# Kernel tuning notes

Hardware: AMD Instinct MI355X
Metric: run time of the kernel (lower is better)

The kernel has to match this reference:

```python
import jax, jax.numpy as jnp
import numpy as np

BLOCK = 8
MAN = 7  # bf16-style mantissa bits


def _ste(x, qx):
    # straight-through estimator: forward = qx, backward = identity
    return x + jax.lax.stop_gradient(qx - x)


def bf16_q(x):
    # fake-quantize to bfloat16 (exp=8, man=7, round-to-nearest)
    return _ste(x, x.astype(jnp.bfloat16).astype(x.dtype))


def bfp_q(x, axis):
    # block floating point: shared exponent per block of 8 along `axis`,
    # 7 mantissa bits relative to floor(log2(max|block|)).
    xm = jnp.moveaxis(x, axis, -1)
    shp = xm.shape
    xb = xm.reshape(shp[:-1] + (shp[-1] // BLOCK, BLOCK))
    maxabs = jnp.max(jnp.abs(xb), axis=-1, keepdims=True)
    _, e = jnp.frexp(maxabs)              # maxabs = m * 2^e, m in [0.5, 1)
    step = jnp.exp2((e - 1 - MAN).astype(x.dtype))  # 2^(floor(log2(maxabs)) - MAN)
    q = jnp.round(xb / step) * step
    q = jnp.where(maxabs > 0, q, jnp.zeros_like(q))
    q = jnp.moveaxis(q.reshape(shp), -1, axis)
    return _ste(x, q)


def _lstm(layer_input, h0, c0, U, V, bih, bhh):
    HS = h0.shape[-1]
    # weight/bias quantization is step-invariant -> hoist out of the scan
    Ut_q = bfp_q(U.T, axis=0)   # [input_size, 4*HS], blocks along dim0
    Vt_q = bfp_q(V.T, axis=0)   # [HS, 4*HS]
    b_q = bf16_q(bih) + bf16_q(bhh)

    def step(carry, x_t):
        h, c = carry
        x_q = bfp_q(x_t, axis=1)          # [B, input_size]
        h_q = bfp_q(h, axis=1)            # [B, HS]
        gates = bf16_q(x_q @ Ut_q + h_q @ Vt_q + b_q)  # [B, 4*HS]
        i_t, f_t, g_t, o_t = jnp.split(gates, 4, axis=1)
        i_t = bf16_q(jax.nn.sigmoid(i_t))
        f_t = bf16_q(jax.nn.sigmoid(f_t))
        g_t = bf16_q(jnp.tanh(g_t))
        o_t = bf16_q(jax.nn.sigmoid(o_t))
        c = bf16_q(f_t * c + i_t * g_t)
        h = bf16_q(o_t * jnp.tanh(c))
        return (h, c), h

    (h_T, c_T), out = jax.lax.scan(step, (h0, c0), layer_input)
    return out, h_T, c_T


def setup_inputs() -> dict:
    key = jax.random.key(0)
    ks = jax.random.split(key, 7)
    S, B, D, HS = 512, 64, 1024, 1024
    return {
        "layer_input": jax.random.normal(ks[0], (S, B, D), jnp.float32),
        "h_t": jax.random.normal(ks[1], (B, HS), jnp.float32),
        "c_t": jax.random.normal(ks[2], (B, HS), jnp.float32),
        "U": jax.random.normal(ks[3], (4 * HS, D), jnp.float32) / np.sqrt(D),
        "V": jax.random.normal(ks[4], (4 * HS, HS), jnp.float32) / np.sqrt(HS),
        "bih": jax.random.normal(ks[5], (4 * HS,), jnp.float32) * 0.1,
        "bhh": jax.random.normal(ks[6], (4 * HS,), jnp.float32) * 0.1,
    }


def reference(layer_input, h_t, c_t, U, V, bih, bhh):
    out, h_T, c_T = _lstm(layer_input, h_t, c_t, U, V, bih, bhh)
    return out, (h_T, c_T)
```

## Files before the change

### kernel.cpp

```cpp
#include <hip/hip_runtime.h>
#include <stdint.h>

typedef __attribute__((ext_vector_type(4))) float f32x4;
typedef __attribute__((ext_vector_type(8))) short bf16x8;
typedef __attribute__((ext_vector_type(4))) int i32x4;
typedef unsigned short ushort_t;
typedef unsigned long long u64;

#define S_LEN 512
#define BATCH 64
#define HSZ   1024
#define G4    4096
#define NWG   256
#define NTHR  256
#define SMEM_BYTES (65536 + 65536 + 32 * 33 * 4)


__device__ __forceinline__ float bf16r(float x) {
    union { float f; uint32_t u; } v; v.f = x;
    v.u = (v.u + 0x7FFFu + ((v.u >> 16) & 1u)) & 0xFFFF0000u;
    return v.f;
}

__device__ __forceinline__ ushort_t bf16bits(float x) {
    union { float f; uint32_t u; } v; v.f = x;
    uint32_t r = v.u + 0x7FFFu + ((v.u >> 16) & 1u);
    return (ushort_t)(r >> 16);
}

__device__ __forceinline__ void bfp8_quant(const float v[8], ushort_t o[8]) {
    float m = 0.f;
    #pragma unroll
    for (int i = 0; i < 8; ++i) m = fmaxf(m, fabsf(v[i]));
    if (m > 0.f) {
        int e;
        (void)frexpf(m, &e);
        float inv_step = ldexpf(1.0f, 8 - e);
        float step     = ldexpf(1.0f, e - 8);
        #pragma unroll
        for (int i = 0; i < 8; ++i) {
            float q = rintf(v[i] * inv_step) * step;
            o[i] = bf16bits(q);
        }
    } else {
        #pragma unroll
        for (int i = 0; i < 8; ++i) o[i] = 0;
    }
}

__device__ __forceinline__ void bfp8_store(const float* __restrict__ src,
                                           ushort_t* __restrict__ dst) {
    float v[8];
    float4 a = ((const float4*)src)[0];
    float4 b = ((const float4*)src)[1];
    v[0]=a.x; v[1]=a.y; v[2]=a.z; v[3]=a.w;
    v[4]=b.x; v[5]=b.y; v[6]=b.z; v[7]=b.w;
    union { ushort_t us[8]; int4 i4; } o;
    bfp8_quant(v, o.us);
    *(int4*)dst = o.i4;
}

__device__ __forceinline__ ushort_t bfp_one(float v, float m) {
    if (!(m > 0.f)) return 0;
    int e;
    (void)frexpf(m, &e);
    float q = rintf(ldexpf(v, 8 - e)) * ldexpf(1.f, e - 8);
    return bf16bits(q);
}


__global__ __launch_bounds__(256) void quant_weights_pack(
    const float* __restrict__ U, const float* __restrict__ V,
    ushort_t* __restrict__ Up, ushort_t* __restrict__ Vp,
    const float* __restrict__ bih, const float* __restrict__ bhh,
    float* __restrict__ bq)
{
    int blk = blockIdx.x * 256 + threadIdx.x;
    int mtx = blk >> 19;
    int r = blk & 524287;
    int n = r >> 7, kb = r & 127;
    int q = n >> 10, j = n & 1023;
    int gslice = j >> 3, jj = j & 7;
    int cc = q * 8 + jj;
    const float* src = (mtx == 0 ? U : V) + (size_t)n * 1024 + kb * 8;
    ushort_t* dst = (mtx == 0 ? Up : Vp) + ((size_t)gslice * 32 + cc) * 1024 + kb * 8;
    bfp8_store(src, dst);
    if (blk < 4096) bq[blk] = bf16r(bih[blk]) + bf16r(bhh[blk]);
}

__global__ __launch_bounds__(256) void init_state(
    const float* __restrict__ h0, const float* __restrict__ c0,
    ushort_t* __restrict__ hq0, float* __restrict__ c_ws)
{
    int idx = blockIdx.x * 256 + threadIdx.x;
    int b = idx >> 7, j0 = (idx & 127) * 8;
    bfp8_store(h0 + (size_t)b * 1024 + j0, hq0 + (size_t)b * 1024 + j0);
    const float4* src = (const float4*)(c0 + (size_t)b * 1024 + j0);
    float4* dst = (float4*)(c_ws + (size_t)b * 1024 + j0);
    dst[0] = src[0]; dst[1] = src[1];
}

__global__ __launch_bounds__(256) void quant_x_all(
    const float* __restrict__ x, ushort_t* __restrict__ xq)
{
    int idx = blockIdx.x * 256 + threadIdx.x;
    int r = idx >> 7, j0 = (idx & 127) * 8;
    bfp8_store(x + (size_t)r * 1024 + j0, xq + (size_t)r * 1024 + j0);
}


__device__ __forceinline__ f32x4 mm32_ll(const char* __restrict__ Alds, int arow,
                                         const char* __restrict__ Blds, int brow,
                                         int lg16, f32x4 acc) {
    const int aswz = (arow & 15) << 4;
    const int bswz = (brow & 15) << 4;
    const char* abase = Alds + arow * 2048;
    const char* bbase = Blds + brow * 2048;
    f32x4 acc2 = {0.f, 0.f, 0.f, 0.f};
    #pragma unroll
    for (int i = 0; i < 32; i += 2) {
        bf16x8 a0 = *(const bf16x8*)(abase + ((i * 64 + lg16) ^ aswz));
        bf16x8 b0 = *(const bf16x8*)(bbase + ((i * 64 + lg16) ^ bswz));
        bf16x8 a1 = *(const bf16x8*)(abase + (((i + 1) * 64 + lg16) ^ aswz));
        bf16x8 b1 = *(const bf16x8*)(bbase + (((i + 1) * 64 + lg16) ^ bswz));
        acc  = __builtin_amdgcn_mfma_f32_16x16x32_bf16(a0, b0, acc,  0, 0, 0);
        acc2 = __builtin_amdgcn_mfma_f32_16x16x32_bf16(a1, b1, acc2, 0, 0, 0);
    }
    return acc + acc2;
}

__device__ __forceinline__ f32x4 mm32_gg(const ushort_t* __restrict__ ap,
                                         const ushort_t* __restrict__ bp,
                                         f32x4 acc) {
    f32x4 acc2 = {0.f, 0.f, 0.f, 0.f};
    #pragma unroll
    for (int c = 0; c < 4; ++c) {
        bf16x8 a[8], b[8];
        #pragma unroll
        for (int i = 0; i < 8; ++i) {
            a[i] = *(const bf16x8*)(ap + (c * 8 + i) * 32);
            b[i] = *(const bf16x8*)(bp + (c * 8 + i) * 32);
        }
        #pragma unroll
        for (int i = 0; i < 8; ++i) {
            if (i & 1) acc2 = __builtin_amdgcn_mfma_f32_16x16x32_bf16(a[i], b[i], acc2, 0, 0, 0);
            else       acc  = __builtin_amdgcn_mfma_f32_16x16x32_bf16(a[i], b[i], acc,  0, 0, 0);
        }
    }
    return acc + acc2;
}

__device__ __forceinline__ f32x4 mm32_xu_g(const float* __restrict__ xrow,
                                           const ushort_t* __restrict__ bp,
                                           f32x4 acc) {
    f32x4 acc2 = {0.f, 0.f, 0.f, 0.f};
    #pragma unroll
    for (int c = 0; c < 4; ++c) {
        float4 f[8][2];
        bf16x8 b[8];
        #pragma unroll
        for (int i = 0; i < 8; ++i) {
            f[i][0] = *(const float4*)(xrow + (c * 8 + i) * 32);
            f[i][1] = *(const float4*)(xrow + (c * 8 + i) * 32 + 4);
            b[i] = *(const bf16x8*)(bp + (c * 8 + i) * 32);
        }
        #pragma unroll
        for (int i = 0; i < 8; ++i) {
            float vv[8] = { f[i][0].x, f[i][0].y, f[i][0].z, f[i][0].w,
                            f[i][1].x, f[i][1].y, f[i][1].z, f[i][1].w };
            union { ushort_t us[8]; bf16x8 v; } aa;
            bfp8_quant(vv, aa.us);
            if (i & 1) acc2 = __builtin_amdgcn_mfma_f32_16x16x32_bf16(aa.v, b[i], acc2, 0, 0, 0);
            else       acc  = __builtin_amdgcn_mfma_f32_16x16x32_bf16(aa.v, b[i], acc,  0, 0, 0);
        }
    }
    return acc + acc2;
}


__global__ __launch_bounds__(256, 1) void lstm_persist(
    const float* __restrict__ x,
    const ushort_t* __restrict__ xq,
    const ushort_t* __restrict__ Up,
    const ushort_t* __restrict__ Vp,
    const float* __restrict__ bq,
    const float* __restrict__ c0_ws,
    ushort_t* __restrict__ hq0, ushort_t* __restrict__ hq1,
    float* __restrict__ out, float* __restrict__ hT, float* __restrict__ cT,
    unsigned int* __restrict__ barrier_cnt)
{
    extern __shared__ char smem[];
    char* Vlds = smem;
    char* Hlds = smem + 65536;
    float* gbuf = (float*)(smem + 131072);

    const int tid = threadIdx.x;
    const int bx = blockIdx.x;
    const int gs = bx & 127;
    const int ms = bx >> 7;
    const int j0 = gs * 8;
    const int lane = tid & 63, wid = tid >> 6;
    const int wm = wid >> 1, wn = wid & 1;
    const int lr = lane & 15, lg = lane >> 4;
    const int lg16 = lg * 16;
    const int brow = wn * 16 + lr;
    const int arow_l = wm * 16 + lr;
    const int arow = ms * 32 + arow_l;
    const bool use_xq = (xq != nullptr);

    {
        const int4* vpg = (const int4*)(Vp + (size_t)gs * 32 * 1024);
        #pragma unroll
        for (int it = 0; it < 16; ++it) {
            int idx = tid + it * 256;
            int row = idx >> 7, kc = idx & 127;
            int off = row * 2048 + ((kc * 16) ^ ((row & 15) << 4));
            *(int4*)(Vlds + off) = vpg[idx];
        }
    }
    __syncthreads();

    const int q_gate = brow >> 3;
    const float bqv = bq[q_gate * 1024 + j0 + (brow & 7)];
    const f32x4 bq4 = {bqv, bqv, bqv, bqv};
    const ushort_t* Ub = Up + ((size_t)gs * 32 + brow) * 1024 + lg * 8;

    const int urow = tid >> 3, ujj = tid & 7;
    const int bg = ms * 32 + urow;
    float c_reg = c0_ws[(size_t)bg * 1024 + j0 + ujj];

    unsigned int* cnt = barrier_cnt + ms * 256;
    unsigned int* myc = cnt + (bx & 7) * 32;

    f32x4 xUacc = use_xq
        ? mm32_gg(xq + (size_t)arow * 1024 + lg * 8, Ub, bq4)
        : mm32_xu_g(x + (size_t)arow * 1024 + lg * 8, Ub, bq4);

    for (int t = 0; t < S_LEN; ++t) {
        const bool doX = (t < S_LEN - 1);
        const ushort_t* hin = (t & 1) ? hq1 : hq0;
        ushort_t* hout = ((t + 1) & 1) ? hq1 : hq0;

        {
            const ushort_t* hsrc = hin + (size_t)ms * 32 * 1024;
            i32x4 hb[16];
            #pragma unroll
            for (int i = 0; i < 16; ++i) {
                asm volatile("global_load_dwordx4 %0, %1, off sc1"
                             : "=v"(hb[i])
                             : "v"(hsrc + ((size_t)(tid + i * 256)) * 8));
            }
            asm volatile("s_waitcnt vmcnt(0)" ::: "memory");
            __builtin_amdgcn_sched_barrier(0);
            #pragma unroll
            for (int i = 0; i < 16; ++i) {
                int c = tid + i * 256;
                int r = c >> 7, kb = (c & 127) * 16;
                *(i32x4*)(Hlds + r * 2048 + (kb ^ ((r & 15) << 4))) = hb[i];
            }
        }
        __syncthreads();

        f32x4 accG = mm32_ll(Hlds, arow_l, Vlds, brow, lg16, xUacc);

        #pragma unroll
        for (int r = 0; r < 4; ++r) {
            float gate = bf16r(accG[r]);
            float sig = 1.f / (1.f + expf(-gate));
            float th  = tanhf(gate);
            float act = bf16r(q_gate == 2 ? th : sig);
            gbuf[(wm * 16 + lg * 4 + r) * 33 + brow] = act;
        }
        __syncthreads();

        float i_t = gbuf[urow * 33 + ujj];
        float f_t = gbuf[urow * 33 + 8 + ujj];
        float g_t = gbuf[urow * 33 + 16 + ujj];
        float o_t = gbuf[urow * 33 + 24 + ujj];
        float cn = bf16r(__fadd_rn(__fmul_rn(f_t, c_reg), __fmul_rn(i_t, g_t)));
        float hn = bf16r(__fmul_rn(o_t, tanhf(cn)));
        c_reg = cn;

        {
            float m = fabsf(hn);
            m = fmaxf(m, __shfl_xor(m, 1));
            m = fmaxf(m, __shfl_xor(m, 2));
            m = fmaxf(m, __shfl_xor(m, 4));
            uint32_t hv = (uint32_t)bfp_one(hn, m);
            uint32_t p1 = __shfl_xor(hv, 1);
            uint32_t w32 = hv | (p1 << 16);
            uint32_t p2 = __shfl_xor(w32, 2);
            u64 w64 = ((u64)p2 << 32) | (u64)w32;
            if ((ujj & 3) == 0) {
                u64* dst = (u64*)(hout + (size_t)bg * 1024 + j0) + (ujj >> 2);
                __hip_atomic_store(dst, w64, __ATOMIC_RELAXED, __HIP_MEMORY_SCOPE_AGENT);
            }
        }

        if (doX) {
            __syncthreads();
            if (tid == 0)
                __hip_atomic_fetch_add(myc, 1u, __ATOMIC_RELAXED, __HIP_MEMORY_SCOPE_AGENT);
        }

        __builtin_nontemporal_store(hn, out + (size_t)t * (BATCH * HSZ) + (size_t)bg * 1024 + j0 + ujj);
        if (t == S_LEN - 1) {
            __builtin_nontemporal_store(hn, hT + (size_t)bg * 1024 + j0 + ujj);
            __builtin_nontemporal_store(cn, cT + (size_t)bg * 1024 + j0 + ujj);
        }

        if (doX) {
            f32x4 accX = use_xq
                ? mm32_gg(xq + (size_t)(t + 1) * (BATCH * HSZ) + (size_t)arow * 1024 + lg * 8, Ub, bq4)
                : mm32_xu_g(x + (size_t)(t + 1) * (BATCH * HSZ) + (size_t)arow * 1024 + lg * 8, Ub, bq4);

            if (wid == 0) {
                const unsigned tgt = 128u * (unsigned)(t + 1);
                while (true) {
                    unsigned v = (lane < 8)
                        ? __hip_atomic_load(cnt + lane * 32, __ATOMIC_RELAXED, __HIP_MEMORY_SCOPE_AGENT)
                        : 0u;
                    #pragma unroll
                    for (int s = 1; s < 64; s <<= 1)
                        v += (unsigned)__shfl_xor((int)v, s);
                    if (v >= tgt) break;
                    __builtin_amdgcn_s_sleep(1);
                }
            }
            __syncthreads();
            xUacc = accX;
        }
    }
}


extern "C" void kernel_launch(void* const* d_in, const int* in_sizes, int n_in,
                              void* d_out, int out_size, void* d_ws, size_t ws_size,
                              hipStream_t stream) {
    const float* x   = (const float*)d_in[0];
    const float* h0  = (const float*)d_in[1];
    const float* c0  = (const float*)d_in[2];
    const float* U   = (const float*)d_in[3];
    const float* V   = (const float*)d_in[4];
    const float* bih = (const float*)d_in[5];
    const float* bhh = (const float*)d_in[6];

    float* out = (float*)d_out;
    float* hT  = out + (size_t)S_LEN * BATCH * HSZ;
    float* cT  = hT + (size_t)BATCH * HSZ;

    char* p = (char*)d_ws;
    ushort_t* Up  = (ushort_t*)p; p += (size_t)G4 * 1024 * 2;
    ushort_t* Vp  = (ushort_t*)p; p += (size_t)G4 * 1024 * 2;
    float* bq     = (float*)p;    p += (size_t)G4 * 4;
    float* c_ws   = (float*)p;    p += (size_t)BATCH * HSZ * 4;
    ushort_t* hq0 = (ushort_t*)p; p += (size_t)BATCH * HSZ * 2;
    ushort_t* hq1 = (ushort_t*)p; p += (size_t)BATCH * HSZ * 2;
    unsigned int* cnt = (unsigned int*)p; p += 2048;
    p = (char*)(((uintptr_t)p + 255) & ~(uintptr_t)255);
    size_t xq_bytes = (size_t)S_LEN * BATCH * HSZ * 2;
    ushort_t* xq = nullptr;
    if ((size_t)(p - (char*)d_ws) + xq_bytes <= ws_size)
        xq = (ushort_t*)p;

    hipMemsetAsync(cnt, 0, 2048, stream);
    hipLaunchKernelGGL(quant_weights_pack, dim3(4096), dim3(256), 0, stream,
                       U, V, Up, Vp, bih, bhh, bq);
    hipLaunchKernelGGL(init_state, dim3(32), dim3(256), 0, stream, h0, c0, hq0, c_ws);
    if (xq)
        hipLaunchKernelGGL(quant_x_all, dim3(16384), dim3(256), 0, stream, x, xq);

    hipFuncSetAttribute(reinterpret_cast<const void*>(lstm_persist),
                        hipFuncAttributeMaxDynamicSharedMemorySize, SMEM_BYTES);

    void* args[] = {
        (void*)&x, (void*)&xq, (void*)&Up, (void*)&Vp, (void*)&bq, (void*)&c_ws,
        (void*)&hq0, (void*)&hq1,
        (void*)&out, (void*)&hT, (void*)&cT, (void*)&cnt
    };
    hipLaunchCooperativeKernel(reinterpret_cast<void*>(lstm_persist),
                               dim3(NWG), dim3(NTHR), args, SMEM_BYTES, stream);
}
```

Measured before the change: 5.586 ms.

## Split persistent LSTM across 512 smaller workgroups and load h directly into registers

Doubles the persistent grid to 512 workgroups of 128 threads, each handling 16 batch rows instead of 32. The per-step h tile is no longer staged through LDS: each lane loads its A fragments straight from global memory into registers. This drops one LDS round trip and one __syncthreads per timestep. In exchange, each workgroup still loads its full V slice, so total V replication doubles, and more workgroups take part in the grid barrier. The barrier-counter indexing (ms = bx>>7) now spans four groups, with the counter buffer enlarged to match.

After: 6.808 ms. 1.22x slower.

```diff
diff --git a/kernel.cpp b/kernel.cpp
--- a/kernel.cpp
+++ b/kernel.cpp
@@ -11,9 +11,9 @@
 #define BATCH 64
 #define HSZ   1024
 #define G4    4096
-#define NWG   256
-#define NTHR  256
-#define SMEM_BYTES (65536 + 65536 + 32 * 33 * 4)
+#define NWG   512
+#define NTHR  128
+#define SMEM_BYTES (65536 + 16 * 33 * 4)
 
 
 __device__ __forceinline__ float bf16r(float x) {
@@ -109,24 +109,36 @@
 }
 
 
-__device__ __forceinline__ f32x4 mm32_ll(const char* __restrict__ Alds, int arow,
-                                         const char* __restrict__ Blds, int brow,
-                                         int lg16, f32x4 acc) {
-    const int aswz = (arow & 15) << 4;
-    const int bswz = (brow & 15) << 4;
-    const char* abase = Alds + arow * 2048;
-    const char* bbase = Blds + brow * 2048;
+__device__ __forceinline__ f32x4 mm32_frag(const bf16x8 a[32],
+                                           const char* __restrict__ bbase,
+                                           int bswz, int lg16, f32x4 acc) {
     f32x4 acc2 = {0.f, 0.f, 0.f, 0.f};
     #pragma unroll
     for (int i = 0; i < 32; i += 2) {
-        bf16x8 a0 = *(const bf16x8*)(abase + ((i * 64 + lg16) ^ aswz));
         bf16x8 b0 = *(const bf16x8*)(bbase + ((i * 64 + lg16) ^ bswz));
-        bf16x8 a1 = *(const bf16x8*)(abase + (((i + 1) * 64 + lg16) ^ aswz));
         bf16x8 b1 = *(const bf16x8*)(bbase + (((i + 1) * 64 + lg16) ^ bswz));
-        acc  = __builtin_amdgcn_mfma_f32_16x16x32_bf16(a0, b0, acc,  0, 0, 0);
-        acc2 = __builtin_amdgcn_mfma_f32_16x16x32_bf16(a1, b1, acc2, 0, 0, 0);
+        acc  = __builtin_amdgcn_mfma_f32_16x16x32_bf16(a[i],     b0, acc,  0, 0, 0);
+        acc2 = __builtin_amdgcn_mfma_f32_16x16x32_bf16(a[i + 1], b1, acc2, 0, 0, 0);
     }
     return acc + acc2;
+}
+
+__device__ __forceinline__ f32x4 mm32_hv(const ushort_t* __restrict__ hrow,
+                                         const char* __restrict__ Blds,
+                                         int brow, int lg16, f32x4 acc) {
+    union { i32x4 i; bf16x8 v; } a[32];
+    #pragma unroll
+    for (int i = 0; i < 32; ++i) {
+        asm volatile("global_load_dwordx4 %0, %1, off sc1"
+                     : "=v"(a[i].i)
+                     : "v"(hrow + i * 32));
+    }
+    asm volatile("s_waitcnt vmcnt(0)" ::: "memory");
+    __builtin_amdgcn_sched_barrier(0);
+    bf16x8 af[32];
+    #pragma unroll
+    for (int i = 0; i < 32; ++i) af[i] = a[i].v;
+    return mm32_frag(af, Blds + brow * 2048, (brow & 15) << 4, lg16, acc);
 }
 
 __device__ __forceinline__ f32x4 mm32_gg(const ushort_t* __restrict__ ap,
@@ -178,7 +190,7 @@
 }
 
 
-__global__ __launch_bounds__(256, 1) void lstm_persist(
+__global__ __launch_bounds__(128, 1) void lstm_persist(
     const float* __restrict__ x,
     const ushort_t* __restrict__ xq,
     const ushort_t* __restrict__ Up,
@@ -191,8 +203,7 @@
 {
     extern __shared__ char smem[];
     char* Vlds = smem;
-    char* Hlds = smem + 65536;
-    float* gbuf = (float*)(smem + 131072);
+    float* gbuf = (float*)(smem + 65536);
 
     const int tid = threadIdx.x;
     const int bx = blockIdx.x;
@@ -200,19 +211,16 @@
     const int ms = bx >> 7;
     const int j0 = gs * 8;
     const int lane = tid & 63, wid = tid >> 6;
-    const int wm = wid >> 1, wn = wid & 1;
+    const int wn = wid;
     const int lr = lane & 15, lg = lane >> 4;
     const int lg16 = lg * 16;
     const int brow = wn * 16 + lr;
-    const int arow_l = wm * 16 + lr;
-    const int arow = ms * 32 + arow_l;
+    const int arow = ms * 16 + lr;
     const bool use_xq = (xq != nullptr);
 
     {
         const int4* vpg = (const int4*)(Vp + (size_t)gs * 32 * 1024);
-        #pragma unroll
-        for (int it = 0; it < 16; ++it) {
-            int idx = tid + it * 256;
+        for (int idx = tid; idx < 4096; idx += NTHR) {
             int row = idx >> 7, kc = idx & 127;
             int off = row * 2048 + ((kc * 16) ^ ((row & 15) << 4));
             *(int4*)(Vlds + off) = vpg[idx];
@@ -226,7 +234,7 @@
     const ushort_t* Ub = Up + ((size_t)gs * 32 + brow) * 1024 + lg * 8;
 
     const int urow = tid >> 3, ujj = tid & 7;
-    const int bg = ms * 32 + urow;
+    const int bg = ms * 16 + urow;
     float c_reg = c0_ws[(size_t)bg * 1024 + j0 + ujj];
 
     unsigned int* cnt = barrier_cnt + ms * 256;
@@ -241,27 +249,7 @@
         const ushort_t* hin = (t & 1) ? hq1 : hq0;
         ushort_t* hout = ((t + 1) & 1) ? hq1 : hq0;
 
-        {
-            const ushort_t* hsrc = hin + (size_t)ms * 32 * 1024;
-            i32x4 hb[16];
-            #pragma unroll
-            for (int i = 0; i < 16; ++i) {
-                asm volatile("global_load_dwordx4 %0, %1, off sc1"
-                             : "=v"(hb[i])
-                             : "v"(hsrc + ((size_t)(tid + i * 256)) * 8));
-            }
-            asm volatile("s_waitcnt vmcnt(0)" ::: "memory");
-            __builtin_amdgcn_sched_barrier(0);
-            #pragma unroll
-            for (int i = 0; i < 16; ++i) {
-                int c = tid + i * 256;
-                int r = c >> 7, kb = (c & 127) * 16;
-                *(i32x4*)(Hlds + r * 2048 + (kb ^ ((r & 15) << 4))) = hb[i];
-            }
-        }
-        __syncthreads();
-
-        f32x4 accG = mm32_ll(Hlds, arow_l, Vlds, brow, lg16, xUacc);
+        f32x4 accG = mm32_hv(hin + (size_t)arow * 1024 + lg * 8, Vlds, brow, lg16, xUacc);
 
         #pragma unroll
         for (int r = 0; r < 4; ++r) {
@@ -269,7 +257,7 @@
             float sig = 1.f / (1.f + expf(-gate));
             float th  = tanhf(gate);
             float act = bf16r(q_gate == 2 ? th : sig);
-            gbuf[(wm * 16 + lg * 4 + r) * 33 + brow] = act;
+            gbuf[(lg * 4 + r) * 33 + brow] = act;
         }
         __syncthreads();
 
@@ -356,14 +344,14 @@
     float* c_ws   = (float*)p;    p += (size_t)BATCH * HSZ * 4;
     ushort_t* hq0 = (ushort_t*)p; p += (size_t)BATCH * HSZ * 2;
     ushort_t* hq1 = (ushort_t*)p; p += (size_t)BATCH * HSZ * 2;
-    unsigned int* cnt = (unsigned int*)p; p += 2048;
+    unsigned int* cnt = (unsigned int*)p; p += 4096;
     p = (char*)(((uintptr_t)p + 255) & ~(uintptr_t)255);
     size_t xq_bytes = (size_t)S_LEN * BATCH * HSZ * 2;
     ushort_t* xq = nullptr;
     if ((size_t)(p - (char*)d_ws) + xq_bytes <= ws_size)
         xq = (ushort_t*)p;
 
-    hipMemsetAsync(cnt, 0, 2048, stream);
+    hipMemsetAsync(cnt, 0, 4096, stream);
     hipLaunchKernelGGL(quant_weights_pack, dim3(4096), dim3(256), 0, stream,
                        U, V, Up, Vp, bih, bhh, bq);
     hipLaunchKernelGGL(init_state, dim3(32), dim3(256), 0, stream, h0, c0, hq0, c_ws);
```
